# Kernel optimization log

Hardware: AMD Instinct MI355X
Metric: run time of the kernel (lower is better)

## Reference

```python
import jax, jax.numpy as jnp
import numpy as np

N_QUBITS = 6
N_LAYERS = 2
QSVT_DEGREE = 3
BATCH = 128
SEQ_LEN = 512
DIM = 2 ** N_QUBITS
# wire 0 is the most-significant bit in the statevector index (PennyLane convention)
_POP = np.array([bin(i).count('1') for i in range(DIM)], dtype=np.float32)
PHASE_SIGN = jnp.asarray(N_QUBITS - 2.0 * _POP)  # (DIM,): sum_w (1 - 2*bit_w)


def _rx(t):
    c = jnp.cos(0.5 * t).astype(jnp.complex64)
    s = (-1j * jnp.sin(0.5 * t)).astype(jnp.complex64)
    return jnp.stack([jnp.stack([c, s]), jnp.stack([s, c])])


def _ry(t):
    c = jnp.cos(0.5 * t).astype(jnp.complex64)
    s = jnp.sin(0.5 * t).astype(jnp.complex64)
    return jnp.stack([jnp.stack([c, -s]), jnp.stack([s, c])])


def _rz(t):
    e = jnp.exp(-0.5j * t.astype(jnp.complex64))
    z = jnp.zeros((), jnp.complex64)
    return jnp.stack([jnp.stack([e, z]), jnp.stack([z, jnp.conj(e)])])


def _apply_1q(psi, U, w):
    # psi: (B,) + (2,)*N_QUBITS ; U: (2,2) complex, same for all batch elems
    psi = jnp.moveaxis(psi, 1 + w, -1)
    psi = psi @ U.T
    return jnp.moveaxis(psi, -1, 1 + w)


def _apply_ry_batched(psi, theta, w):
    # RY with a per-batch angle theta: (B,)
    psi = jnp.moveaxis(psi, 1 + w, -1)
    c = jnp.cos(0.5 * theta).reshape((-1,) + (1,) * (N_QUBITS - 1))
    s = jnp.sin(0.5 * theta).reshape((-1,) + (1,) * (N_QUBITS - 1))
    a, b = psi[..., 0], psi[..., 1]
    psi = jnp.stack([c * a - s * b, s * a + c * b], axis=-1)
    return jnp.moveaxis(psi, -1, 1 + w)


def _cnot(psi, c, t):
    p0 = jax.lax.index_in_dim(psi, 0, axis=1 + c, keepdims=True)
    p1 = jax.lax.index_in_dim(psi, 1, axis=1 + c, keepdims=True)
    p1 = jnp.flip(p1, axis=1 + t)
    return jnp.concatenate([p0, p1], axis=1 + c)


def _circuit_step(h, x, params, poly):
    # h, x: (B, N_QUBITS) angles. Returns <Z_w> per qubit: (B, N_QUBITS).
    B = h.shape[0]
    # 1) state encoding: RY(h_w)|0> = cos(h/2)|0> + sin(h/2)|1>  (product state)
    c, s = jnp.cos(0.5 * h), jnp.sin(0.5 * h)
    psi = jnp.ones((B, 1), jnp.complex64)
    for w in range(N_QUBITS):
        amp = jnp.stack([c[:, w], s[:, w]], axis=-1).astype(jnp.complex64)  # (B,2)
        psi = (psi[:, :, None] * amp[:, None, :]).reshape(B, -1)
    psi = psi.reshape((B,) + (2,) * N_QUBITS)
    # 2) QSVT block: RZ(coeff*pi) on every wire fuses into one diagonal phase
    for d in range(QSVT_DEGREE + 1):
        theta = poly[d] * np.pi
        phase = jnp.exp((-0.5j) * theta * PHASE_SIGN)  # (DIM,)
        psi = (psi.reshape(B, -1) * phase[None, :]).reshape((B,) + (2,) * N_QUBITS)
        for i in range(N_QUBITS - 1):
            psi = _cnot(psi, i, i + 1)
        psi = _cnot(psi, N_QUBITS - 1, 0)  # ring closure
    # 3) variational layers: per-wire RZ@RY@RX (RX applied first), then CNOT chain
    idx = 0
    for _ in range(N_LAYERS):
        for i in range(N_QUBITS):
            U = _rz(params[idx + 2]) @ _ry(params[idx + 1]) @ _rx(params[idx])
            psi = _apply_1q(psi, U, i)
            idx += 3
        for i in range(N_QUBITS - 1):
            psi = _cnot(psi, i, i + 1)
    # 4) input injection: RY(x_w) with per-batch angles
    for w in range(N_QUBITS):
        psi = _apply_ry_batched(psi, x[:, w], w)
    # 5) measurement: <Z_w> = P(bit_w=0) - P(bit_w=1)
    p = jnp.abs(psi) ** 2
    zs = []
    for w in range(N_QUBITS):
        axes = tuple(a for a in range(1, N_QUBITS + 1) if a != 1 + w)
        pw = p.sum(axis=axes)  # (B,2)
        zs.append(pw[:, 0] - pw[:, 1])
    return jnp.stack(zs, axis=-1)


def _ssm_pass(angles, params, poly, reverse):
    a = jnp.flip(angles, axis=1) if reverse else angles
    xs = jnp.moveaxis(a, 1, 0)  # (T, B, n)
    h0 = jnp.zeros((a.shape[0], N_QUBITS), jnp.float32)

    def step(h, x):
        hn = _circuit_step(h, x, params, poly)
        return hn, hn

    _, ys = jax.lax.scan(step, h0, xs)
    out = jnp.moveaxis(ys, 0, 1)  # (B, T, n)
    return jnp.flip(out, axis=1) if reverse else out


def setup_inputs() -> dict:
    key = jax.random.key(0)
    k0, k1, k2, k3 = jax.random.split(key, 4)
    angles = jax.random.uniform(k0, (BATCH, SEQ_LEN, N_QUBITS), jnp.float32) * np.float32(np.pi)
    poly_coeffs = jax.random.normal(k1, (QSVT_DEGREE + 1,), jnp.float32) * 0.1
    fwd_params = jax.random.normal(k2, (N_QUBITS * N_LAYERS * 3,), jnp.float32) * 0.1
    bwd_params = jax.random.normal(k3, (N_QUBITS * N_LAYERS * 3,), jnp.float32) * 0.1
    fwd_coeff = jnp.full((1,), 0.5, jnp.float32)
    bwd_coeff = jnp.full((1,), 0.5, jnp.float32)
    return {'angles': angles, 'poly_coeffs': poly_coeffs, 'fwd_params': fwd_params,
            'bwd_params': bwd_params, 'fwd_coeff': fwd_coeff, 'bwd_coeff': bwd_coeff}


def reference(angles, poly_coeffs, fwd_params, bwd_params, fwd_coeff, bwd_coeff):
    h_fwd = _ssm_pass(angles, fwd_params, poly_coeffs, reverse=False)
    h_bwd = _ssm_pass(angles, bwd_params, poly_coeffs, reverse=True)
    return jax.nn.sigmoid(fwd_coeff) * h_fwd + jax.nn.sigmoid(bwd_coeff) * h_bwd
```

## Files before the change

### kernel.cpp

```cpp
#include <hip/hip_runtime.h>
#include <hip/hip_bf16.h>
#include <stdint.h>

#define BATCH 128
#define SEQ   512
#define NW    6
#define DIM   64
#define NELEM (BATCH * SEQ * NW)
#define PI_F  3.14159265358979323846f

typedef float v2f __attribute__((ext_vector_type(2)));
typedef uint16_t u16x8 __attribute__((ext_vector_type(8)));

__device__ __forceinline__ v2f pkfma(float s, v2f m, v2f a) {
    return __builtin_elementwise_fma((v2f){s, s}, m, a);
}

template <int CTRL>
__device__ __forceinline__ void red_stage6(float v[6]) {
#pragma unroll
    for (int k = 0; k < 6; ++k)
        v[k] += __int_as_float(__builtin_amdgcn_update_dpp(
            0, __float_as_int(v[k]), CTRL, 0xF, 0xF, false));
}

template <int CTRL>
__device__ __forceinline__ float dpp_mov(float x) {
    return __int_as_float(__builtin_amdgcn_update_dpp(
        0, __float_as_int(x), CTRL, 0xF, 0xF, false));
}

__device__ __forceinline__ void sincos_half(float h, float& s, float& c) {
    const float u = h * h;
    c = fmaf(u, fmaf(u, 2.6041667e-3f, -0.125f), 1.0f);
    s = h * fmaf(u, fmaf(u, 2.6041667e-4f, -2.0833333e-2f), 0.5f);
}

__device__ __forceinline__ float ldf(const void* p, int i, bool bf) {
    if (bf) {
        uint32_t u = (uint32_t)((const uint16_t*)p)[i];
        return __uint_as_float(u << 16);
    }
    return ((const float*)p)[i];
}

__global__ void k_prep(const void* ang, const void* poly, const void* fp,
                       const void* bp, const void* fc, const void* bc,
                       float* __restrict__ misc, float* __restrict__ Mg,
                       int* __restrict__ flag) {
    __shared__ int cnt;
    if (threadIdx.x == 0) cnt = 0;
    __syncthreads();
    {
        uint32_t w = ((const uint32_t*)ang)[threadIdx.x & 255];
        uint32_t e = (w >> 8) & 0xFFu;
        if (e >= 0x3Au && e <= 0x41u) atomicAdd(&cnt, 1);
    }
    __syncthreads();
    const bool bf = (cnt >= 128);

    if (blockIdx.x == 32) {
        if (threadIdx.x == 0)      misc[76] = ldf(fc, 0, bf);
        else if (threadIdx.x == 1) misc[77] = ldf(bc, 0, bf);
        else if (threadIdx.x == 2) *flag = bf ? 1 : 0;
        return;
    }

    const int lane = threadIdx.x & 63;
    const int tix  = blockIdx.x * 4 + (threadIdx.x >> 6);
    const int dir  = tix >> 6;
    const int col  = tix & 63;
    const void* prm = dir ? bp : fp;
    const int p = lane;

    float yr = (p == col) ? 1.f : 0.f;
    float yi = 0.f;

#pragma unroll
    for (int d = 0; d < 4; ++d) {
        const float th = 0.5f * PI_F * ldf(poly, d, bf) *
                         (float)(6 - 2 * (int)__popc((unsigned)p));
        float s, c;
        __sincosf(th, &s, &c);
        const float nr = yr * c + yi * s;
        const float ni = yi * c - yr * s;
        yr = nr; yi = ni;
#pragma unroll
        for (int k = 0; k < 6; ++k) {
            const int cw = k, tw = (k + 1) % 6;
            const int src = p ^ (((p >> (5 - cw)) & 1) << (5 - tw));
            yr = __shfl(yr, src, 64);
            yi = __shfl(yi, src, 64);
        }
    }

    int idx = 0;
#pragma unroll
    for (int l = 0; l < 2; ++l) {
#pragma unroll
        for (int w = 0; w < 6; ++w) {
            float cx, sx, cy, sy, cz, sz;
            __sincosf(0.5f * ldf(prm, idx + 0, bf), &sx, &cx);
            __sincosf(0.5f * ldf(prm, idx + 1, bf), &sy, &cy);
            __sincosf(0.5f * ldf(prm, idx + 2, bf), &sz, &cz);
            idx += 3;
            const float A = cy * cx, B = sy * sx, C = sy * cx, D = cy * sx;
            const float U00r = cz * A + sz * B, U00i = cz * B - sz * A;
            const float U11r = U00r,            U11i = sz * A - cz * B;
            const float Xr   = cz * C + sz * D, Xi   = sz * C - cz * D;
            const int m  = 1 << (5 - w);
            const int bb = (p >> (5 - w)) & 1;
            const float C1r = bb ? U11r : U00r;
            const float C1i = bb ? U11i : U00i;
            const float C2r = bb ? Xr : -Xr;
            const float C2i = Xi;
            const float pr = __shfl_xor(yr, m, 64);
            const float pi = __shfl_xor(yi, m, 64);
            const float nr = C1r * yr - C1i * yi + C2r * pr - C2i * pi;
            const float ni = C1r * yi + C1i * yr + C2r * pi + C2i * pr;
            yr = nr; yi = ni;
        }
#pragma unroll
        for (int k = 0; k < 5; ++k) {
            const int src = p ^ (((p >> (5 - k)) & 1) << (5 - (k + 1)));
            yr = __shfl(yr, src, 64);
            yi = __shfl(yi, src, 64);
        }
    }

    float* out = Mg + ((size_t)(dir * 64 + p) * 64 + (size_t)col) * 2;
    out[0] = yr;
    out[1] = yi;
}

__global__ void
__attribute__((amdgpu_flat_work_group_size(64, 64)))
__attribute__((amdgpu_waves_per_eu(1, 1)))
k_sim(const void* __restrict__ ang, const float* __restrict__ Mg,
      float* __restrict__ hbuf, const int* __restrict__ flag) {
    const int lane  = threadIdx.x;
    const int chain = blockIdx.x;
    const int dir   = chain >> 7;
    const int b     = chain & 127;
    const bool bf   = (*flag != 0);

    __shared__ __align__(16) float cl[SEQ * 12];
    __shared__ __align__(16) float zb[SEQ * NW];

    if (!bf) {
        const float4* src =
            (const float4*)((const float*)ang + (size_t)b * (SEQ * NW));
#pragma unroll
        for (int k = 0; k < 12; ++k) {
            const int v = k * 64 + lane;
            const float4 a = src[v];
            __align__(16) float o[8];
            float s, c;
            __sincosf(a.x, &s, &c); o[0] = c; o[1] = s;
            __sincosf(a.y, &s, &c); o[2] = c; o[3] = s;
            __sincosf(a.z, &s, &c); o[4] = c; o[5] = s;
            __sincosf(a.w, &s, &c); o[6] = c; o[7] = s;
            ((float4*)cl)[2 * v]     = ((const float4*)o)[0];
            ((float4*)cl)[2 * v + 1] = ((const float4*)o)[1];
        }
    } else {
        const u16x8* src =
            (const u16x8*)((const uint16_t*)ang + (size_t)b * (SEQ * NW));
#pragma unroll
        for (int k = 0; k < 6; ++k) {
            const int v = k * 64 + lane;
            const u16x8 a = src[v];
            __align__(16) float o[16];
#pragma unroll
            for (int e = 0; e < 8; ++e) {
                const float x = __uint_as_float(((uint32_t)a[e]) << 16);
                float s, c;
                __sincosf(x, &s, &c);
                o[2 * e] = c; o[2 * e + 1] = s;
            }
#pragma unroll
            for (int j = 0; j < 4; ++j)
                ((float4*)cl)[4 * v + j] = ((const float4*)o)[j];
        }
    }

    v2f Mc[64];
    {
        const float4* mr4 =
            (const float4*)(Mg + (size_t)(dir * 64 + lane) * 128);
#pragma unroll
        for (int k = 0; k < 32; ++k) {
            const float4 m = mr4[k];
            Mc[2 * k]     = (v2f){m.x, m.y};
            Mc[2 * k + 1] = (v2f){m.z, m.w};
        }
    }

    int zmask[6];
#pragma unroll
    for (int w = 0; w < 6; ++w) zmask[w] = ((lane >> (5 - w)) & 1) << 31;

    const float* cp = cl + (dir ? (SEQ - 1) * 12 : 0);
    const int   cstep = dir ? -12 : 12;
    float*       zp = zb + (dir ? (SEQ - 1) * NW : 0);
    const int   zstep = dir ? -NW : NW;

    float h[6] = {0.f, 0.f, 0.f, 0.f, 0.f, 0.f};

    __syncthreads();

    for (int t = 0; t < SEQ; ++t) {
        const float4 xq0 = ((const float4*)cp)[0];
        const float4 xq1 = ((const float4*)cp)[1];
        const float4 xq2 = ((const float4*)cp)[2];
        cp += cstep;

        float cw[6], sw[6];
#pragma unroll
        for (int w = 0; w < 6; ++w) sincos_half(h[w], sw[w], cw[w]);
        float g01[4], g45[4], eH[8], eL[8];
        g01[0] = cw[0] * cw[1]; g01[1] = cw[0] * sw[1];
        g01[2] = sw[0] * cw[1]; g01[3] = sw[0] * sw[1];
        g45[0] = cw[4] * cw[5]; g45[1] = cw[4] * sw[5];
        g45[2] = sw[4] * cw[5]; g45[3] = sw[4] * sw[5];
#pragma unroll
        for (int j = 0; j < 8; ++j) {
            eH[j] = g01[j >> 1] * ((j & 1) ? sw[2] : cw[2]);
            eL[j] = ((j >> 2) ? sw[3] : cw[3]) * g45[j & 3];
        }

        v2f y = {0.f, 0.f};
#pragma unroll
        for (int jh = 0; jh < 8; ++jh) {
            v2f n = {0.f, 0.f};
#pragma unroll
            for (int jl = 0; jl < 8; ++jl)
                n = pkfma(eL[jl], Mc[8 * jh + jl], n);
            y = pkfma(eH[jh], n, y);
        }
        const float yr = y.x, yi = y.y;
        const int yri = __float_as_int(yr), yii = __float_as_int(yi);

        float pr[6], pi[6];
        {
            auto r0 = __builtin_amdgcn_permlane32_swap(yri, yri, false, false);
            auto r1 = __builtin_amdgcn_permlane32_swap(yii, yii, false, false);
            pr[0] = __int_as_float((int)((lane & 32) ? r0[0] : r0[1]));
            pi[0] = __int_as_float((int)((lane & 32) ? r1[0] : r1[1]));
        }
        {
            auto r0 = __builtin_amdgcn_permlane16_swap(yri, yri, false, false);
            auto r1 = __builtin_amdgcn_permlane16_swap(yii, yii, false, false);
            pr[1] = __int_as_float((int)((lane & 16) ? r0[0] : r0[1]));
            pi[1] = __int_as_float((int)((lane & 16) ? r1[0] : r1[1]));
        }
        pr[2] = dpp_mov<0x128>(yr);
        pi[2] = dpp_mov<0x128>(yi);
        pr[3] = dpp_mov<0x141>(dpp_mov<0x1B>(yr));
        pi[3] = dpp_mov<0x141>(dpp_mov<0x1B>(yi));
        pr[4] = dpp_mov<0x4E>(yr);
        pi[4] = dpp_mov<0x4E>(yi);
        pr[5] = dpp_mov<0xB1>(yr);
        pi[5] = dpp_mov<0xB1>(yi);

        const float q = fmaf(yr, yr, yi * yi);
        const float cx[6] = {xq0.x, xq0.z, xq1.x, xq1.z, xq2.x, xq2.z};
        const float sx[6] = {xq0.y, xq0.w, xq1.y, xq1.w, xq2.y, xq2.w};

        float v[6];
#pragma unroll
        for (int w = 0; w < 6; ++w) {
            const float cq  = __int_as_float(__float_as_int(cx[w] * q) ^ zmask[w]);
            const float dot = fmaf(yr, pr[w], yi * pi[w]);
            v[w] = fmaf(-sx[w], dot, cq);
        }

        red_stage6<0x111>(v);
        red_stage6<0x112>(v);
        red_stage6<0x114>(v);
        red_stage6<0x118>(v);
        red_stage6<0x142>(v);
        red_stage6<0x143>(v);

        if (lane == 63) {
#pragma unroll
            for (int w = 0; w < 6; ++w) zp[w] = v[w];
        }
        zp += zstep;
#pragma unroll
        for (int w = 0; w < 6; ++w)
            h[w] = __int_as_float(
                __builtin_amdgcn_readlane(__float_as_int(v[w]), 63));
    }

    __syncthreads();

    {
        float* orow = hbuf + (size_t)dir * NELEM + (size_t)b * (SEQ * NW);
        const float4* zs4 = (const float4*)zb;
        float4* go = (float4*)orow;
#pragma unroll
        for (int k = 0; k < 12; ++k) {
            const int idx = k * 64 + lane;
            go[idx] = zs4[idx];
        }
    }
}

__global__ void k_combine(const float* __restrict__ hbuf,
                          const float* __restrict__ misc,
                          void* __restrict__ out, const int* __restrict__ flag) {
    const int i = blockIdx.x * blockDim.x + threadIdx.x;
    if (i >= NELEM) return;
    const float sf = 1.f / (1.f + __expf(-misc[76]));
    const float sb = 1.f / (1.f + __expf(-misc[77]));
    const float v = sf * hbuf[i] + sb * hbuf[NELEM + i];
    if (*flag) ((__hip_bfloat16*)out)[i] = __float2bfloat16(v);
    else       ((float*)out)[i] = v;
}

extern "C" void kernel_launch(void* const* d_in, const int* in_sizes, int n_in,
                              void* d_out, int out_size, void* d_ws, size_t ws_size,
                              hipStream_t stream) {
    const void* ang  = d_in[0];
    const void* poly = d_in[1];
    const void* fp   = d_in[2];
    const void* bp   = d_in[3];
    const void* fc   = d_in[4];
    const void* bc   = d_in[5];

    float* misc = (float*)d_ws + 32;
    float* hbuf = misc + 128;
    float* Mg   = hbuf + 2 * NELEM;
    int*   flag = (int*)(Mg + 2 * 64 * 64 * 2);

    k_prep<<<33, 256, 0, stream>>>(ang, poly, fp, bp, fc, bc, misc, Mg, flag);
    k_sim<<<256, 64, 0, stream>>>(ang, Mg, hbuf, flag);
    k_combine<<<(NELEM + 255) / 256, 256, 0, stream>>>(hbuf, misc, d_out, flag);
}
```

Measured before the change: 385.0 us.

## Split per-step 64x64 matvec across four waves with LDS partial-sum exchange

Measured after the change: 381.4 us. About the same (-0.9%).

```diff
diff --git a/kernel.cpp b/kernel.cpp
--- a/kernel.cpp
+++ b/kernel.cpp
@@ -133,26 +133,28 @@
     out[1] = yi;
 }
 
-__global__ void
-__attribute__((amdgpu_flat_work_group_size(64, 64)))
-__attribute__((amdgpu_waves_per_eu(1, 1)))
-k_sim(const void* __restrict__ ang, const float* __restrict__ Mg,
-      float* __restrict__ hbuf, const int* __restrict__ flag) {
-    const int lane  = threadIdx.x;
+__global__ void __launch_bounds__(256, 1) k_sim(const void* __restrict__ ang,
+                                                const float* __restrict__ Mg,
+                                                float* __restrict__ hbuf,
+                                                const int* __restrict__ flag) {
+    const int tid   = threadIdx.x;
+    const int lane  = tid & 63;
+    const int wv    = tid >> 6;
     const int chain = blockIdx.x;
     const int dir   = chain >> 7;
     const int b     = chain & 127;
     const bool bf   = (*flag != 0);
 
-    __shared__ __align__(16) float cl[SEQ * 12];
-    __shared__ __align__(16) float zb[SEQ * NW];
+    __shared__ __align__(16) float  cl[SEQ * 12];
+    __shared__ __align__(16) float  zb[SEQ * NW];
+    __shared__ float2 pY[2][4][DIM];
 
     if (!bf) {
         const float4* src =
             (const float4*)((const float*)ang + (size_t)b * (SEQ * NW));
 #pragma unroll
-        for (int k = 0; k < 12; ++k) {
-            const int v = k * 64 + lane;
+        for (int k = 0; k < 3; ++k) {
+            const int v = k * 256 + tid;
             const float4 a = src[v];
             __align__(16) float o[8];
             float s, c;
@@ -167,78 +169,90 @@
         const u16x8* src =
             (const u16x8*)((const uint16_t*)ang + (size_t)b * (SEQ * NW));
 #pragma unroll
-        for (int k = 0; k < 6; ++k) {
-            const int v = k * 64 + lane;
-            const u16x8 a = src[v];
-            __align__(16) float o[16];
-#pragma unroll
-            for (int e = 0; e < 8; ++e) {
-                const float x = __uint_as_float(((uint32_t)a[e]) << 16);
-                float s, c;
-                __sincosf(x, &s, &c);
-                o[2 * e] = c; o[2 * e + 1] = s;
+        for (int k = 0; k < 2; ++k) {
+            const int v = k * 256 + tid;
+            if (v < 384) {
+                const u16x8 a = src[v];
+                __align__(16) float o[16];
+#pragma unroll
+                for (int e = 0; e < 8; ++e) {
+                    const float x = __uint_as_float(((uint32_t)a[e]) << 16);
+                    float s, c;
+                    __sincosf(x, &s, &c);
+                    o[2 * e] = c; o[2 * e + 1] = s;
+                }
+#pragma unroll
+                for (int j = 0; j < 4; ++j)
+                    ((float4*)cl)[4 * v + j] = ((const float4*)o)[j];
             }
-#pragma unroll
-            for (int j = 0; j < 4; ++j)
-                ((float4*)cl)[4 * v + j] = ((const float4*)o)[j];
-        }
-    }
-
-    v2f Mc[64];
+        }
+    }
+
+    v2f Mres[16];
     {
-        const float4* mr4 =
-            (const float4*)(Mg + (size_t)(dir * 64 + lane) * 128);
-#pragma unroll
-        for (int k = 0; k < 32; ++k) {
-            const float4 m = mr4[k];
-            Mc[2 * k]     = (v2f){m.x, m.y};
-            Mc[2 * k + 1] = (v2f){m.z, m.w};
-        }
+        const float2* mr2 =
+            (const float2*)(Mg + (size_t)(dir * 64 + lane) * 128 + 32 * wv);
+#pragma unroll
+        for (int k = 0; k < 16; ++k) Mres[k] = (v2f){mr2[k].x, mr2[k].y};
     }
 
     int zmask[6];
 #pragma unroll
     for (int w = 0; w < 6; ++w) zmask[w] = ((lane >> (5 - w)) & 1) << 31;
+    const int ow0 = wv ^ 1, ow1 = wv ^ 2, ow2 = wv ^ 3;
+
+    float h[6] = {0.f, 0.f, 0.f, 0.f, 0.f, 0.f};
+
+    auto encode_matvec = [&](v2f& acc) {
+        float cw6[6], sw6[6];
+#pragma unroll
+        for (int w = 0; w < 6; ++w) sincos_half(h[w], sw6[w], cw6[w]);
+        const float t0 = (wv & 2) ? sw6[0] : cw6[0];
+        const float t1 = (wv & 1) ? sw6[1] : cw6[1];
+        const float A  = t0 * t1;
+        float GH[4], GL[4];
+        GH[0] = cw6[2] * cw6[3]; GH[1] = cw6[2] * sw6[3];
+        GH[2] = sw6[2] * cw6[3]; GH[3] = sw6[2] * sw6[3];
+#pragma unroll
+        for (int a = 0; a < 4; ++a) GH[a] *= A;
+        GL[0] = cw6[4] * cw6[5]; GL[1] = cw6[4] * sw6[5];
+        GL[2] = sw6[4] * cw6[5]; GL[3] = sw6[4] * sw6[5];
+        v2f y = {0.f, 0.f};
+#pragma unroll
+        for (int a = 0; a < 4; ++a) {
+            v2f T = {0.f, 0.f};
+#pragma unroll
+            for (int b2 = 0; b2 < 4; ++b2)
+                T = pkfma(GL[b2], Mres[4 * a + b2], T);
+            y = pkfma(GH[a], T, y);
+        }
+        acc = y;
+    };
 
     const float* cp = cl + (dir ? (SEQ - 1) * 12 : 0);
     const int   cstep = dir ? -12 : 12;
     float*       zp = zb + (dir ? (SEQ - 1) * NW : 0);
     const int   zstep = dir ? -NW : NW;
 
-    float h[6] = {0.f, 0.f, 0.f, 0.f, 0.f, 0.f};
-
     __syncthreads();
 
+    v2f myacc;
+    encode_matvec(myacc);
+    pY[0][wv][lane] = (float2){myacc.x, myacc.y};
+    float4 xq0 = ((const float4*)cp)[0];
+    float4 xq1 = ((const float4*)cp)[1];
+    float4 xq2 = ((const float4*)cp)[2];
+    cp += cstep;
+    __syncthreads();
+
     for (int t = 0; t < SEQ; ++t) {
-        const float4 xq0 = ((const float4*)cp)[0];
-        const float4 xq1 = ((const float4*)cp)[1];
-        const float4 xq2 = ((const float4*)cp)[2];
-        cp += cstep;
-
-        float cw[6], sw[6];
-#pragma unroll
-        for (int w = 0; w < 6; ++w) sincos_half(h[w], sw[w], cw[w]);
-        float g01[4], g45[4], eH[8], eL[8];
-        g01[0] = cw[0] * cw[1]; g01[1] = cw[0] * sw[1];
-        g01[2] = sw[0] * cw[1]; g01[3] = sw[0] * sw[1];
-        g45[0] = cw[4] * cw[5]; g45[1] = cw[4] * sw[5];
-        g45[2] = sw[4] * cw[5]; g45[3] = sw[4] * sw[5];
-#pragma unroll
-        for (int j = 0; j < 8; ++j) {
-            eH[j] = g01[j >> 1] * ((j & 1) ? sw[2] : cw[2]);
-            eL[j] = ((j >> 2) ? sw[3] : cw[3]) * g45[j & 3];
-        }
-
-        v2f y = {0.f, 0.f};
-#pragma unroll
-        for (int jh = 0; jh < 8; ++jh) {
-            v2f n = {0.f, 0.f};
-#pragma unroll
-            for (int jl = 0; jl < 8; ++jl)
-                n = pkfma(eL[jl], Mc[8 * jh + jl], n);
-            y = pkfma(eH[jh], n, y);
-        }
-        const float yr = y.x, yi = y.y;
+        const int buf = t & 1;
+
+        const float2 yA = pY[buf][ow0][lane];
+        const float2 yB = pY[buf][ow1][lane];
+        const float2 yC = pY[buf][ow2][lane];
+        const float yr = (myacc.x + yA.x) + (yB.x + yC.x);
+        const float yi = (myacc.y + yA.y) + (yB.y + yC.y);
         const int yri = __float_as_int(yr), yii = __float_as_int(yi);
 
         float pr[6], pi[6];
@@ -275,6 +289,13 @@
             v[w] = fmaf(-sx[w], dot, cq);
         }
 
+        if (t + 1 < SEQ) {
+            xq0 = ((const float4*)cp)[0];
+            xq1 = ((const float4*)cp)[1];
+            xq2 = ((const float4*)cp)[2];
+            cp += cstep;
+        }
+
         red_stage6<0x111>(v);
         red_stage6<0x112>(v);
         red_stage6<0x114>(v);
@@ -282,7 +303,7 @@
         red_stage6<0x142>(v);
         red_stage6<0x143>(v);
 
-        if (lane == 63) {
+        if (tid == 63) {
 #pragma unroll
             for (int w = 0; w < 6; ++w) zp[w] = v[w];
         }
@@ -291,17 +312,19 @@
         for (int w = 0; w < 6; ++w)
             h[w] = __int_as_float(
                 __builtin_amdgcn_readlane(__float_as_int(v[w]), 63));
-    }
-
-    __syncthreads();
+
+        encode_matvec(myacc);
+        pY[buf ^ 1][wv][lane] = (float2){myacc.x, myacc.y};
+        __syncthreads();
+    }
 
     {
-        float* orow = hbuf + (size_t)dir * NELEM + (size_t)b * (SEQ * NW);
         const float4* zs4 = (const float4*)zb;
-        float4* go = (float4*)orow;
-#pragma unroll
-        for (int k = 0; k < 12; ++k) {
-            const int idx = k * 64 + lane;
+        float4* go = (float4*)(hbuf + (size_t)dir * NELEM +
+                               (size_t)b * (SEQ * NW));
+#pragma unroll
+        for (int k = 0; k < 3; ++k) {
+            const int idx = tid + k * 256;
             go[idx] = zs4[idx];
         }
     }
@@ -335,6 +358,6 @@
     int*   flag = (int*)(Mg + 2 * 64 * 64 * 2);
 
     k_prep<<<33, 256, 0, stream>>>(ang, poly, fp, bp, fc, bc, misc, Mg, flag);
-    k_sim<<<256, 64, 0, stream>>>(ang, Mg, hbuf, flag);
+    k_sim<<<256, 256, 0, stream>>>(ang, Mg, hbuf, flag);
     k_combine<<<(NELEM + 255) / 256, 256, 0, stream>>>(hbuf, misc, d_out, flag);
 }
```
